# Kernel optimization log

Hardware: AMD Instinct MI355X
Metric: run time of the kernel (lower is better)

## Reference

```python
import jax, jax.numpy as jnp
import numpy as np
from math import sqrt
from itertools import product

NUM_CLASSES = 21
TOP_K = 200
VAR = (0.1, 0.2)
CONF_THRESH = 0.01
NMS_THRESH = 0.45
EPS = 1e-6
BATCH = 32


def make_priors():
    # Exact SSD300 PriorBox generation (8732 boxes, cx/cy/w/h in [0,1])
    image_size = 300
    feature_maps = [38, 19, 10, 5, 3, 1]
    steps = [8, 16, 32, 64, 100, 300]
    min_sizes = [30, 60, 111, 162, 213, 264]
    max_sizes = [60, 111, 162, 213, 264, 315]
    ars = [[2], [2, 3], [2, 3], [2, 3], [2], [2]]
    mean = []
    for k, f in enumerate(feature_maps):
        for i, j in product(range(f), repeat=2):
            f_k = image_size / steps[k]
            cx = (j + 0.5) / f_k
            cy = (i + 0.5) / f_k
            s_k = min_sizes[k] / image_size
            mean += [cx, cy, s_k, s_k]
            s_kp = sqrt(s_k * (max_sizes[k] / image_size))
            mean += [cx, cy, s_kp, s_kp]
            for ar in ars[k]:
                mean += [cx, cy, s_k * sqrt(ar), s_k / sqrt(ar)]
                mean += [cx, cy, s_k / sqrt(ar), s_k * sqrt(ar)]
    pri = np.asarray(mean, np.float32).reshape(-1, 4)
    return np.clip(pri, 0.0, 1.0)


def setup_inputs() -> dict:
    key = jax.random.key(0)
    k1, k2 = jax.random.split(key)
    priors = jnp.asarray(make_priors())  # [8732, 4]
    P = priors.shape[0]
    loc = jax.random.normal(k1, (BATCH, P, 4), jnp.float32) * 0.5
    conf = jax.random.normal(k2, (BATCH, P, NUM_CLASSES), jnp.float32)
    return {"loc": loc, "conf": conf, "priors": priors}


def _decode(loc, priors):
    # calc_predicted_bboxes: cx/cy offset + clamped log-w/h, then corner clamp [0,1]
    pri = jnp.clip(priors, EPS, None)
    cx = pri[:, 0] + loc[:, 0] * VAR[0] * pri[:, 2]
    cy = pri[:, 1] + loc[:, 1] * VAR[0] * pri[:, 3]
    lw = jnp.clip(loc[:, 2] * VAR[1], -4.0, 4.0)
    lh = jnp.clip(loc[:, 3] * VAR[1], -4.0, 4.0)
    w = pri[:, 2] * jnp.exp(lw)
    h = pri[:, 3] * jnp.exp(lh)
    return jnp.stack([
        jnp.clip(cx - w / 2, 0.0, 1.0), jnp.clip(cy - h / 2, 0.0, 1.0),
        jnp.clip(cx + w / 2, 0.0, 1.0), jnp.clip(cy + h / 2, 0.0, 1.0)], axis=1)


def _iou_matrix(b):  # b: [K,4] -> [K,K]
    area = (b[:, 2] - b[:, 0]) * (b[:, 3] - b[:, 1])
    lt = jnp.maximum(b[:, None, :2], b[None, :, :2])
    rb = jnp.minimum(b[:, None, 2:], b[None, :, 2:])
    wh = jnp.clip(rb - lt, 0.0)
    inter = wh[..., 0] * wh[..., 1]
    union = area[:, None] + area[None, :] - inter
    return inter / jnp.maximum(union, 1e-12)


def _per_class(boxes, scores):
    # boxes [P,4], scores [P] -> [TOP_K, 5] rows of [score, x1, y1, x2, y2]
    valid = (scores > CONF_THRESH) \
        & (boxes[:, 2] > boxes[:, 0] + EPS) & (boxes[:, 3] > boxes[:, 1] + EPS)
    masked = jnp.where(valid, scores, -1.0)
    top_s, top_i = jax.lax.top_k(masked, TOP_K)  # highest-score candidates
    top_b = boxes[top_i]
    top_valid = top_s > CONF_THRESH  # invalid padded entries have score -1
    ious = _iou_matrix(top_b)
    pos = jnp.arange(TOP_K)

    def body(i, alive):
        keep_i = alive[i] & top_valid[i]
        suppress = keep_i & (ious[i] > NMS_THRESH) & (pos > i)
        return alive & ~suppress

    alive = jax.lax.fori_loop(0, TOP_K, body, jnp.ones(TOP_K, bool))
    keep = alive & top_valid
    # compact kept detections to the front, preserving score order
    order = jnp.argsort(jnp.where(keep, pos, TOP_K + pos))
    rows = jnp.concatenate([top_s[:, None], top_b], axis=1)[order]
    return jnp.where(keep[order][:, None], rows, 0.0)


def reference(loc, conf, priors):
    probs = jax.nn.softmax(jnp.clip(conf, -100.0, 100.0), axis=-1)  # [B,P,C]
    boxes = jax.vmap(_decode, in_axes=(0, None))(loc, priors)       # [B,P,4]

    def per_image(b, p):
        fg = jax.vmap(_per_class, in_axes=(None, 1))(b, p[:, 1:])   # [C-1,K,5]
        return jnp.concatenate([jnp.zeros((1, TOP_K, 5), b.dtype), fg], axis=0)

    return jax.vmap(per_image)(boxes, probs)  # [B, C, K, 5]
```

## Files before the change

kernel.cpp:

```cpp
#include <hip/hip_runtime.h>
#include <cstdint>

#define P_BOX 8732
#define NBOX_TOTAL 279424
#define BATCH 32
#define NCLS 21
#define NFG 20
#define TOPK 200
#define NTH 256
#define NCH 9
#define CAND_CAP 512
#define NBKT 2048
#define NORM 0xBC23D70Bu
#define LIM (1u << 26)
#define CONF_F4 1466976

typedef unsigned long long u64;

__device__ __forceinline__ uint32_t score_key(float m) {
  uint32_t b = __float_as_uint(m);
  return (b & 0x80000000u) ? ~b : (b | 0x80000000u);
}
__device__ __forceinline__ float key_score(uint32_t k) {
  uint32_t b = (k & 0x80000000u) ? (k ^ 0x80000000u) : ~k;
  return __uint_as_float(b);
}

__device__ __forceinline__ float4 decode_box(const float4 pr, const float4 lc) {
  float px = fmaxf(pr.x, 1e-6f), py = fmaxf(pr.y, 1e-6f);
  float pw = fmaxf(pr.z, 1e-6f), ph = fmaxf(pr.w, 1e-6f);
  float cx = px + lc.x * 0.1f * pw;
  float cy = py + lc.y * 0.1f * ph;
  float lw = fminf(fmaxf(lc.z * 0.2f, -4.0f), 4.0f);
  float lh = fminf(fmaxf(lc.w * 0.2f, -4.0f), 4.0f);
  float w = pw * expf(lw);
  float h = ph * expf(lh);
  float4 r;
  r.x = fminf(fmaxf(cx - 0.5f * w, 0.0f), 1.0f);
  r.y = fminf(fmaxf(cy - 0.5f * h, 0.0f), 1.0f);
  r.z = fminf(fmaxf(cx + 0.5f * w, 0.0f), 1.0f);
  r.w = fminf(fmaxf(cy + 0.5f * h, 0.0f), 1.0f);
  return r;
}

__global__ __launch_bounds__(256) void prep_kernel(
    const float* __restrict__ loc, const float* __restrict__ conf,
    const float* __restrict__ priors, uint32_t* __restrict__ keys) {
  __shared__ float s_conf[256 * 21];
  const int t = threadIdx.x;
  const int blk = blockIdx.x;
  const float4* cf4 = (const float4*)conf;
  size_t base4 = (size_t)blk * 1344;
#pragma unroll
  for (int i = t; i < 1344; i += 256) {
    size_t g4 = base4 + i;
    if (g4 < CONF_F4) ((float4*)s_conf)[i] = cf4[g4];
  }
  __syncthreads();
  int g = blk * 256 + t;
  if (g >= NBOX_TOTAL) return;
  int b = g / P_BOX, p = g - b * P_BOX;
  float x[NCLS];
  float mx = -1e30f;
#pragma unroll
  for (int i = 0; i < NCLS; ++i) {
    float v = fminf(fmaxf(s_conf[t * 21 + i], -100.0f), 100.0f);
    x[i] = v;
    mx = fmaxf(mx, v);
  }
  float s = 0.0f;
#pragma unroll
  for (int i = 0; i < NCLS; ++i) {
    x[i] = expf(x[i] - mx);
    s += x[i];
  }
  float4 bx = decode_box(((const float4*)priors)[p], ((const float4*)loc)[g]);
  bool bok = (bx.z > bx.x + 1e-6f) && (bx.w > bx.y + 1e-6f);
#pragma unroll
  for (int ci = 1; ci < NCLS; ++ci) {
    float sc = x[ci] / s;
    float m = (bok && sc > 0.01f) ? sc : -1.0f;
    keys[((size_t)(b * NFG) + (ci - 1)) * P_BOX + p] = score_key(m) - NORM;
  }
}

__device__ __forceinline__ int cnt_ge(const uint32_t* kv, uint32_t X) {
  int n = 0;
#pragma unroll
  for (int j = 0; j < NCH * 4; ++j) n += (kv[j] >= X && kv[j] < LIM) ? 1 : 0;
  return n;
}
__device__ __forceinline__ int cnt_eq_idx(const uint32_t* kv, int t, uint32_t T, uint32_t I) {
  int n = 0;
#pragma unroll
  for (int ch = 0; ch < NCH; ++ch) {
#pragma unroll
    for (int e = 0; e < 4; ++e) {
      int p = ch * 1024 + t * 4 + e;
      n += (kv[ch * 4 + e] == T && (uint32_t)(P_BOX - p) >= I) ? 1 : 0;
    }
  }
  return n;
}

__device__ __forceinline__ int block_count(int v, int t, int* s_cnt, int& it) {
#pragma unroll
  for (int o = 32; o > 0; o >>= 1) v += __shfl_down(v, o, 64);
  int slot = it % 3;
  if (t == 0) s_cnt[(it + 1) % 3] = 0;
  if ((t & 63) == 0) atomicAdd(&s_cnt[slot], v);
  __syncthreads();
  int r = s_cnt[slot];
  ++it;
  return r;
}

__device__ __forceinline__ int3 select_bucket(const int* s_hist, int* s_S,
                                              int* s_wt, int* s_res, int need,
                                              int t) {
  const int BPT = NBKT / NTH;
  int base = t * BPT;
  int ps = 0;
#pragma unroll
  for (int i = 0; i < BPT; ++i) ps += s_hist[base + i];
  int l = t & 63, w = t >> 6;
  int v = ps;
#pragma unroll
  for (int off = 1; off < 64; off <<= 1) {
    int o = __shfl_down(v, off, 64);
    v += (l + off < 64) ? o : 0;
  }
  if (l == 0) s_wt[w] = v;
  __syncthreads();
  int hi = 0;
#pragma unroll
  for (int w2 = 0; w2 < NTH / 64; ++w2) hi += (w2 > w) ? s_wt[w2] : 0;
  int S = v + hi;
  s_S[t] = S;
  __syncthreads();
  if (t == 0 && s_S[0] < need) {
    s_res[0] = 0; s_res[1] = s_S[0]; s_res[2] = 0;
  } else if (s_S[t] >= need && (t == NTH - 1 || s_S[t + 1] < need)) {
    int suf = (t == NTH - 1) ? 0 : s_S[t + 1];
    int B = base, M = 0;
    for (int j = base + BPT - 1; j >= base; --j) {
      suf += s_hist[j];
      if (suf >= need) { B = j; M = suf; break; }
    }
    s_res[0] = B; s_res[1] = M; s_res[2] = M - s_hist[B];
  }
  __syncthreads();
  return make_int3(s_res[0], s_res[1], s_res[2]);
}

template <bool USE_WS>
__global__ __launch_bounds__(256) void task_kernel(
    const float* __restrict__ loc, const float* __restrict__ conf,
    const float* __restrict__ priors, const uint32_t* __restrict__ keys,
    float* __restrict__ out) {
  const int t = threadIdx.x;
  const int task = blockIdx.x;
  const int b = task / NCLS, c = task - b * NCLS;
  float* ob = out + (size_t)task * TOPK * 5;

  if (c == 0) {
    float4 z = make_float4(0.f, 0.f, 0.f, 0.f);
    for (int i = t; i < TOPK * 5 / 4; i += NTH) ((float4*)ob)[i] = z;
    return;
  }
  const int ft = b * NFG + (c - 1);

  __shared__ alignas(16) int s_hist[NBKT];
  __shared__ alignas(16) u64 s_cand[CAND_CAP];
  __shared__ u64 s_sel[TOPK];
  __shared__ float4 s_box[TOPK];
  __shared__ float s_area[TOPK];
  __shared__ float s_score[TOPK];
  __shared__ u64 s_alive[4];
  __shared__ u64 s_nxt[4];
  __shared__ int s_chg;
  __shared__ short s_kept[TOPK];
  __shared__ int s_wt[NTH / 64];
  __shared__ int s_res[3];
  __shared__ int s_cnt[3];
  __shared__ int s_m;
  int* s_S = (int*)s_cand;
  float* s_out = (float*)s_hist;

  if (t == 0) { s_cnt[0] = 0; s_cnt[1] = 0; s_cnt[2] = 0; s_m = 0; }
  for (int i = t; i < NBKT; i += NTH) s_hist[i] = 0;

  uint32_t kv[NCH * 4];
  if (USE_WS) {
    const uint4* kp = (const uint4*)(keys + (size_t)ft * P_BOX);
#pragma unroll
    for (int ch = 0; ch < 8; ++ch) {
      uint4 v = kp[ch * 256 + t];
      kv[ch * 4 + 0] = v.x; kv[ch * 4 + 1] = v.y;
      kv[ch * 4 + 2] = v.z; kv[ch * 4 + 3] = v.w;
    }
    if (t < 135) {
      uint4 v = kp[2048 + t];
      kv[32] = v.x; kv[33] = v.y; kv[34] = v.z; kv[35] = v.w;
    } else {
      kv[32] = LIM; kv[33] = LIM; kv[34] = LIM; kv[35] = LIM;
    }
  } else {
    for (int ch = 0; ch < NCH; ++ch) {
      int p0 = ch * 1024 + 4 * t;
#pragma unroll
      for (int e = 0; e < 4; ++e) {
        int p = p0 + e;
        uint32_t k = LIM;
        if (p < P_BOX) {
          const float* cf = conf + (size_t)(b * P_BOX + p) * NCLS;
          float x[NCLS];
          float mx = -1e30f;
#pragma unroll
          for (int i = 0; i < NCLS; ++i) {
            float v = fminf(fmaxf(cf[i], -100.0f), 100.0f);
            x[i] = v;
            mx = fmaxf(mx, v);
          }
          float ssum = 0.0f, ec = 0.0f;
#pragma unroll
          for (int i = 0; i < NCLS; ++i) {
            float ex = expf(x[i] - mx);
            ssum += ex;
            if (i == c) ec = ex;
          }
          float sc = ec / ssum;
          float4 bx = decode_box(((const float4*)priors)[p],
                                 ((const float4*)loc)[(size_t)b * P_BOX + p]);
          bool valid = (sc > 0.01f) && (bx.z > bx.x + 1e-6f) && (bx.w > bx.y + 1e-6f);
          k = score_key(valid ? sc : -1.0f) - NORM;
        }
        kv[ch * 4 + e] = k;
      }
    }
  }
  __syncthreads();

#pragma unroll
  for (int j = 0; j < NCH * 4; ++j)
    if (kv[j] < LIM) atomicAdd(&s_hist[kv[j] >> 15], 1);
  __syncthreads();
  int3 r1 = select_bucket(s_hist, s_S, s_wt, s_res, TOPK, t);
  uint32_t Tp = (uint32_t)r1.x << 15;
  int M = r1.y;
  bool ex = false;
  uint32_t Tex = 0, I = 0;

  if (M > CAND_CAP) {
    uint32_t B1 = (uint32_t)r1.x;
    int above1 = r1.z;
    __syncthreads();
    for (int i = t; i < NBKT; i += NTH) s_hist[i] = 0;
    __syncthreads();
#pragma unroll
    for (int j = 0; j < NCH * 4; ++j)
      if (kv[j] < LIM && (kv[j] >> 15) == B1)
        atomicAdd(&s_hist[(kv[j] >> 4) & (NBKT - 1)], 1);
    __syncthreads();
    int3 r2 = select_bucket(s_hist, s_S, s_wt, s_res, TOPK - above1, t);
    Tp = (B1 << 15) + ((uint32_t)r2.x << 4);
    M = above1 + r2.y;
    if (M > CAND_CAP) {
      int it = 0;
      uint32_t lo = Tp, hi = LIM;
      while (hi - lo > 1) {
        uint32_t mid = lo + ((hi - lo) >> 1);
        int cnt = block_count(cnt_ge(kv, mid), t, s_cnt, it);
        if (cnt >= TOPK) lo = mid; else hi = mid;
      }
      Tex = lo;
      int G = block_count(cnt_ge(kv, Tex + 1), t, s_cnt, it);
      int R = TOPK - G;
      uint32_t lo2 = 1, hi2 = P_BOX + 1;
      while (hi2 - lo2 > 1) {
        uint32_t mid = lo2 + ((hi2 - lo2) >> 1);
        int cnt = block_count(cnt_eq_idx(kv, t, Tex, mid), t, s_cnt, it);
        if (cnt >= R) lo2 = mid; else hi2 = mid;
      }
      I = lo2;
      ex = true;
    }
  }
  __syncthreads();

#pragma unroll
  for (int ch = 0; ch < NCH; ++ch) {
#pragma unroll
    for (int e = 0; e < 4; ++e) {
      uint32_t k = kv[ch * 4 + e];
      if (k < LIM) {
        int p = ch * 1024 + 4 * t + e;
        bool take = ex ? (k > Tex || (k == Tex && (uint32_t)(P_BOX - p) >= I))
                       : (k >= Tp);
        if (take) {
          int ix = atomicAdd(&s_m, 1);
          if (ix < CAND_CAP) s_cand[ix] = ((u64)k << 32) | (uint32_t)(P_BOX - p);
        }
      }
    }
  }
  __syncthreads();
  M = min(s_m, CAND_CAP);
  int nsel = min(M, TOPK);

  for (int ci = t; ci < M; ci += NTH) {
    u64 mine = s_cand[ci];
    int r = 0;
    int j = 0;
    for (; j + 8 <= M; j += 8) {
      u64 a0 = s_cand[j + 0], a1 = s_cand[j + 1], a2 = s_cand[j + 2],
          a3 = s_cand[j + 3], a4 = s_cand[j + 4], a5 = s_cand[j + 5],
          a6 = s_cand[j + 6], a7 = s_cand[j + 7];
      r += (a0 > mine) + (a1 > mine) + (a2 > mine) + (a3 > mine) +
           (a4 > mine) + (a5 > mine) + (a6 > mine) + (a7 > mine);
    }
    for (; j < M; ++j) r += (s_cand[j] > mine) ? 1 : 0;
    if (r < TOPK) s_sel[r] = mine;
  }
  __syncthreads();

  if (t < TOPK) {
    if (t < nsel) {
      u64 w = s_sel[t];
      uint32_t k = (uint32_t)(w >> 32);
      int p = P_BOX - (int)(uint32_t)(w & 0xFFFFFFFFull);
      float4 bx = decode_box(((const float4*)priors)[p],
                             ((const float4*)loc)[(size_t)b * P_BOX + p]);
      s_box[t] = bx;
      s_area[t] = (bx.z - bx.x) * (bx.w - bx.y);
      s_score[t] = key_score(k + NORM);
    } else {
      s_box[t] = make_float4(0.f, 0.f, 0.f, 0.f);
      s_area[t] = 0.f;
      s_score[t] = 0.f;
    }
  }
  __syncthreads();

  float4 bj = make_float4(0.f, 0.f, 0.f, 0.f);
  float aj = 0.f;
  const bool validj = (t < nsel);
  if (validj) { bj = s_box[t]; aj = s_area[t]; }
  u64 cm0 = 0, cm1 = 0, cm2 = 0, cm3 = 0;
#pragma unroll
  for (int band = 0; band < 4; ++band) {
    const int base = band * 64;
    const int iend = min(base + 64, nsel);
    u64 w = 0;
#pragma unroll 4
    for (int i = base; i < iend; ++i) {
      float4 bi = s_box[i];
      float ai = s_area[i];
      float lx = fmaxf(bi.x, bj.x), ly = fmaxf(bi.y, bj.y);
      float rx = fminf(bi.z, bj.z), ry = fminf(bi.w, bj.w);
      float iw = fmaxf(rx - lx, 0.0f), ih = fmaxf(ry - ly, 0.0f);
      float inter = iw * ih;
      float uni = ai + aj - inter;
      float iou = inter / fmaxf(uni, 1e-12f);
      bool sup = (i < t) && validj && (iou > 0.45f);
      w |= ((u64)sup) << (i - base);
    }
    if (band == 0) cm0 = w; else if (band == 1) cm1 = w;
    else if (band == 2) cm2 = w; else cm3 = w;
  }

  int q0 = nsel, q1 = nsel - 64, q2 = nsel - 128, q3 = nsel - 192;
  u64 v0 = q0 >= 64 ? ~0ull : (q0 <= 0 ? 0ull : ((1ull << q0) - 1));
  u64 v1 = q1 >= 64 ? ~0ull : (q1 <= 0 ? 0ull : ((1ull << q1) - 1));
  u64 v2 = q2 >= 64 ? ~0ull : (q2 <= 0 ? 0ull : ((1ull << q2) - 1));
  u64 v3 = q3 >= 64 ? ~0ull : (q3 <= 0 ? 0ull : ((1ull << q3) - 1));
  if (t == 0) { s_alive[0] = v0; s_alive[1] = v1; s_alive[2] = v2; s_alive[3] = v3; }
  __syncthreads();

  for (int it2 = 0; it2 <= TOPK; ++it2) {
    u64 a0 = s_alive[0], a1 = s_alive[1], a2 = s_alive[2], a3 = s_alive[3];
    bool sup = ((cm0 & a0) | (cm1 & a1) | (cm2 & a2) | (cm3 & a3)) != 0ull;
    bool na = validj && !sup;
    u64 m = __ballot(na);
    if ((t & 63) == 0) s_nxt[t >> 6] = m;
    __syncthreads();
    if (t == 0) {
      s_chg = (s_nxt[0] != a0) || (s_nxt[1] != a1) ||
              (s_nxt[2] != a2) || (s_nxt[3] != a3);
      s_alive[0] = s_nxt[0]; s_alive[1] = s_nxt[1];
      s_alive[2] = s_nxt[2]; s_alive[3] = s_nxt[3];
    }
    __syncthreads();
    if (!s_chg) break;
  }

  u64 w0 = s_alive[0], w1 = s_alive[1], w2 = s_alive[2], w3 = s_alive[3];
  int pc0 = __popcll(w0), pc01 = pc0 + __popcll(w1), pc012 = pc01 + __popcll(w2);
  int nk = pc012 + __popcll(w3);
  if (t < nsel) {
    int word = t >> 6, bit = t & 63;
    u64 wt = (word == 0) ? w0 : (word == 1) ? w1 : (word == 2) ? w2 : w3;
    if ((wt >> bit) & 1ull) {
      int base = (word == 0) ? 0 : (word == 1) ? pc0 : (word == 2) ? pc01 : pc012;
      int r = base + __popcll(wt & ((1ull << bit) - 1ull));
      s_kept[r] = (short)t;
    }
  }
  __syncthreads();

  if (t < TOPK) {
    float o0 = 0.f, o1 = 0.f, o2 = 0.f, o3 = 0.f, o4 = 0.f;
    if (t < nk) {
      int j = s_kept[t];
      o0 = s_score[j];
      float4 bx = s_box[j];
      o1 = bx.x; o2 = bx.y; o3 = bx.z; o4 = bx.w;
    }
    s_out[t * 5 + 0] = o0; s_out[t * 5 + 1] = o1; s_out[t * 5 + 2] = o2;
    s_out[t * 5 + 3] = o3; s_out[t * 5 + 4] = o4;
  }
  __syncthreads();
  for (int i = t; i < TOPK * 5 / 4; i += NTH)
    ((float4*)ob)[i] = ((float4*)s_out)[i];
}

extern "C" void kernel_launch(void* const* d_in, const int* in_sizes, int n_in,
                              void* d_out, int out_size, void* d_ws, size_t ws_size,
                              hipStream_t stream) {
  (void)in_sizes;
  (void)n_in;
  (void)out_size;
  const float* loc = (const float*)d_in[0];
  const float* conf = (const float*)d_in[1];
  const float* priors = (const float*)d_in[2];
  float* out = (float*)d_out;

  size_t keys_bytes = (size_t)BATCH * NFG * P_BOX * sizeof(uint32_t);
  if (ws_size >= keys_bytes) {
    uint32_t* keys = (uint32_t*)d_ws;
    int nprep = (NBOX_TOTAL + 255) / 256;
    prep_kernel<<<nprep, 256, 0, stream>>>(loc, conf, priors, keys);
    task_kernel<true><<<BATCH * NCLS, NTH, 0, stream>>>(loc, conf, priors, keys, out);
  } else {
    task_kernel<false><<<BATCH * NCLS, NTH, 0, stream>>>(loc, conf, priors, nullptr, out);
  }
}
```

Baseline: 133.2 us.

## Aggregate candidate atomics per wavefront and halve NMS fixpoint barriers

Candidate compaction now does one ballot per element and a single shared atomicAdd per wavefront, instead of one atomic per selected element. The IoU mask loop now stops at the thread's own index, which drops the lower-triangle work and the per-iteration predicate. The NMS fixed-point loop keeps the alive masks in registers and double-buffers the shared ballot words, so each iteration needs one barrier instead of two plus a serial thread-0 update. The risks are extra ballot and shuffle instructions in compaction and a divergent trip count in the IoU loop.

New measurement: 127.7 us. 4.1% less time.

```diff
diff --git a/kernel.cpp b/kernel.cpp
--- a/kernel.cpp
+++ b/kernel.cpp
@@ -176,9 +176,7 @@
   __shared__ float4 s_box[TOPK];
   __shared__ float s_area[TOPK];
   __shared__ float s_score[TOPK];
-  __shared__ u64 s_alive[4];
-  __shared__ u64 s_nxt[4];
-  __shared__ int s_chg;
+  __shared__ u64 s_nxt[2][4];
   __shared__ short s_kept[TOPK];
   __shared__ int s_wt[NTH / 64];
   __shared__ int s_res[3];
@@ -288,18 +286,29 @@
   }
   __syncthreads();
 
-#pragma unroll
-  for (int ch = 0; ch < NCH; ++ch) {
-#pragma unroll
-    for (int e = 0; e < 4; ++e) {
-      uint32_t k = kv[ch * 4 + e];
-      if (k < LIM) {
+  {
+    const int lane = t & 63;
+#pragma unroll
+    for (int ch = 0; ch < NCH; ++ch) {
+#pragma unroll
+      for (int e = 0; e < 4; ++e) {
+        uint32_t k = kv[ch * 4 + e];
         int p = ch * 1024 + 4 * t + e;
-        bool take = ex ? (k > Tex || (k == Tex && (uint32_t)(P_BOX - p) >= I))
-                       : (k >= Tp);
-        if (take) {
-          int ix = atomicAdd(&s_m, 1);
-          if (ix < CAND_CAP) s_cand[ix] = ((u64)k << 32) | (uint32_t)(P_BOX - p);
+        bool take = (k < LIM) &&
+                    (ex ? (k > Tex || (k == Tex && (uint32_t)(P_BOX - p) >= I))
+                        : (k >= Tp));
+        u64 m = __ballot(take);
+        if (m) {
+          int leader = __ffsll((long long)m) - 1;
+          int base = 0;
+          if (lane == leader) base = atomicAdd(&s_m, __popcll(m));
+          base = __shfl(base, leader, 64);
+          if (take) {
+            int pre = __popcll(m & ((1ull << lane) - 1ull));
+            int ix = base + pre;
+            if (ix < CAND_CAP)
+              s_cand[ix] = ((u64)k << 32) | (uint32_t)(P_BOX - p);
+          }
         }
       }
     }
@@ -346,11 +355,12 @@
   float aj = 0.f;
   const bool validj = (t < nsel);
   if (validj) { bj = s_box[t]; aj = s_area[t]; }
+  const int tcl = min(t, nsel);
   u64 cm0 = 0, cm1 = 0, cm2 = 0, cm3 = 0;
 #pragma unroll
   for (int band = 0; band < 4; ++band) {
     const int base = band * 64;
-    const int iend = min(base + 64, nsel);
+    const int iend = min(base + 64, tcl);
     u64 w = 0;
 #pragma unroll 4
     for (int i = base; i < iend; ++i) {
@@ -362,7 +372,7 @@
       float inter = iw * ih;
       float uni = ai + aj - inter;
       float iou = inter / fmaxf(uni, 1e-12f);
-      bool sup = (i < t) && validj && (iou > 0.45f);
+      bool sup = (iou > 0.45f);
       w |= ((u64)sup) << (i - base);
     }
     if (band == 0) cm0 = w; else if (band == 1) cm1 = w;
@@ -370,36 +380,29 @@
   }
 
   int q0 = nsel, q1 = nsel - 64, q2 = nsel - 128, q3 = nsel - 192;
-  u64 v0 = q0 >= 64 ? ~0ull : (q0 <= 0 ? 0ull : ((1ull << q0) - 1));
-  u64 v1 = q1 >= 64 ? ~0ull : (q1 <= 0 ? 0ull : ((1ull << q1) - 1));
-  u64 v2 = q2 >= 64 ? ~0ull : (q2 <= 0 ? 0ull : ((1ull << q2) - 1));
-  u64 v3 = q3 >= 64 ? ~0ull : (q3 <= 0 ? 0ull : ((1ull << q3) - 1));
-  if (t == 0) { s_alive[0] = v0; s_alive[1] = v1; s_alive[2] = v2; s_alive[3] = v3; }
-  __syncthreads();
-
+  u64 a0 = q0 >= 64 ? ~0ull : (q0 <= 0 ? 0ull : ((1ull << q0) - 1));
+  u64 a1 = q1 >= 64 ? ~0ull : (q1 <= 0 ? 0ull : ((1ull << q1) - 1));
+  u64 a2 = q2 >= 64 ? ~0ull : (q2 <= 0 ? 0ull : ((1ull << q2) - 1));
+  u64 a3 = q3 >= 64 ? ~0ull : (q3 <= 0 ? 0ull : ((1ull << q3) - 1));
   for (int it2 = 0; it2 <= TOPK; ++it2) {
-    u64 a0 = s_alive[0], a1 = s_alive[1], a2 = s_alive[2], a3 = s_alive[3];
     bool sup = ((cm0 & a0) | (cm1 & a1) | (cm2 & a2) | (cm3 & a3)) != 0ull;
     bool na = validj && !sup;
     u64 m = __ballot(na);
-    if ((t & 63) == 0) s_nxt[t >> 6] = m;
+    int buf = it2 & 1;
+    if ((t & 63) == 0) s_nxt[buf][t >> 6] = m;
     __syncthreads();
-    if (t == 0) {
-      s_chg = (s_nxt[0] != a0) || (s_nxt[1] != a1) ||
-              (s_nxt[2] != a2) || (s_nxt[3] != a3);
-      s_alive[0] = s_nxt[0]; s_alive[1] = s_nxt[1];
-      s_alive[2] = s_nxt[2]; s_alive[3] = s_nxt[3];
-    }
-    __syncthreads();
-    if (!s_chg) break;
-  }
-
-  u64 w0 = s_alive[0], w1 = s_alive[1], w2 = s_alive[2], w3 = s_alive[3];
-  int pc0 = __popcll(w0), pc01 = pc0 + __popcll(w1), pc012 = pc01 + __popcll(w2);
-  int nk = pc012 + __popcll(w3);
+    u64 n0 = s_nxt[buf][0], n1 = s_nxt[buf][1];
+    u64 n2 = s_nxt[buf][2], n3 = s_nxt[buf][3];
+    bool chg = (n0 != a0) || (n1 != a1) || (n2 != a2) || (n3 != a3);
+    a0 = n0; a1 = n1; a2 = n2; a3 = n3;
+    if (!chg) break;
+  }
+
+  int pc0 = __popcll(a0), pc01 = pc0 + __popcll(a1), pc012 = pc01 + __popcll(a2);
+  int nk = pc012 + __popcll(a3);
   if (t < nsel) {
     int word = t >> 6, bit = t & 63;
-    u64 wt = (word == 0) ? w0 : (word == 1) ? w1 : (word == 2) ? w2 : w3;
+    u64 wt = (word == 0) ? a0 : (word == 1) ? a1 : (word == 2) ? a2 : a3;
     if ((wt >> bit) & 1ull) {
       int base = (word == 0) ? 0 : (word == 1) ? pc0 : (word == 2) ? pc01 : pc012;
       int r = base + __popcll(wt & ((1ull << bit) - 1ull));
```
